# Kernel optimization log

Hardware: AMD Instinct MI355X
Metric: run time of the kernel (lower is better)

The kernel has to match this reference:

```python
import jax, jax.numpy as jnp
import numpy as np

B, S, H, OUT, STEPS = 64, 1024, 512, 256, 32


def setup_inputs() -> dict:
    key = jax.random.key(0)
    ks = jax.random.split(key, 10)
    s = 0.02
    return {
        "encoder_outputs": jax.random.normal(ks[0], (B, S, H), jnp.float32),
        "hidden": jax.random.normal(ks[1], (B, H), jnp.float32),
        # Attention: nn.Linear(2H, 1)
        "attn_w": jax.random.normal(ks[2], (2 * H,), jnp.float32) * s,
        "attn_b": jax.random.normal(ks[3], (1,), jnp.float32) * s,
        # LSTMCell(OUT + H, H): torch gate order i, f, g, o
        "w_ih": jax.random.normal(ks[4], (4 * H, OUT + H), jnp.float32) * s,
        "w_hh": jax.random.normal(ks[5], (4 * H, H), jnp.float32) * s,
        "b_ih": jax.random.normal(ks[6], (4 * H,), jnp.float32) * s,
        "b_hh": jax.random.normal(ks[7], (4 * H,), jnp.float32) * s,
        # fc: nn.Linear(H, OUT)
        "fc_w": jax.random.normal(ks[8], (OUT, H), jnp.float32) * s,
        "fc_b": jax.random.normal(ks[9], (OUT,), jnp.float32) * s,
    }


def reference(encoder_outputs, hidden, attn_w, attn_b, w_ih, w_hh, b_ih, b_hh, fc_w, fc_b):
    # Split attention weight: Linear(concat(enc, hid)) == enc@wa_e + hid@wa_d + b
    wa_e, wa_d = attn_w[:H], attn_w[H:]
    # encoder contribution to attention energy is step-invariant: [B, S]
    enc_energy = jnp.einsum("bsh,h->bs", encoder_outputs, wa_e) + attn_b[0]
    bias = b_ih + b_hh  # [4H]

    def step(carry, _):
        h, c, dec_in = carry
        # Bahdanau-style energy and context
        energy = enc_energy + (h @ wa_d)[:, None]          # [B, S]
        weights = jax.nn.softmax(energy, axis=1)
        context = jnp.einsum("bs,bsh->bh", weights, encoder_outputs)
        # LSTMCell (torch gate order i, f, g, o)
        x = jnp.concatenate([dec_in, context], axis=1)     # [B, OUT+H]
        gates = x @ w_ih.T + h @ w_hh.T + bias             # [B, 4H]
        i, f, g, o = jnp.split(gates, 4, axis=1)
        c_new = jax.nn.sigmoid(f) * c + jax.nn.sigmoid(i) * jnp.tanh(g)
        h_new = jax.nn.sigmoid(o) * jnp.tanh(c_new)
        dec_new = h_new @ fc_w.T + fc_b                    # [B, OUT]
        return (h_new, c_new, dec_new), dec_new

    dec0 = jnp.zeros((encoder_outputs.shape[0], fc_w.shape[0]), encoder_outputs.dtype)
    c0 = jnp.zeros_like(hidden)
    _, outs = jax.lax.scan(step, (hidden, c0, dec0), None, length=STEPS)
    return jnp.transpose(outs, (1, 0, 2))  # [B, STEPS, OUT]
```

## Files before the change

### kernel.cpp

```cpp
#include <hip/hip_runtime.h>
#include <math.h>

#define B 64
#define S 1024
#define H 512
#define OUT 256
#define STEPS 32
#define NG 2048
#define X 768

typedef __attribute__((ext_vector_type(8))) short short8;
typedef __attribute__((ext_vector_type(4))) short s16x4;
typedef __attribute__((ext_vector_type(4))) float f32x4;
typedef __attribute__((ext_vector_type(4))) unsigned u32x4;

__device__ __forceinline__ float sigf(float x) { return 1.0f / (1.0f + __expf(-x)); }
__device__ __forceinline__ float tanhf_fast(float x) {
  return 2.0f / (1.0f + __expf(-2.0f * x)) - 1.0f;
}

__device__ __forceinline__ short f2bf(float x) {
  union { float f; unsigned u; } a; a.f = x;
  unsigned r = a.u + 0x7fffu + ((a.u >> 16) & 1u);
  return (short)(r >> 16);
}
__device__ __forceinline__ float bf2f(short s) {
  union { unsigned u; float f; } a; a.u = ((unsigned)(unsigned short)s) << 16;
  return a.f;
}

__device__ __forceinline__ unsigned load_u32_cg(const unsigned* p) {
  unsigned r;
  asm volatile("global_load_dword %0, %1, off sc0 sc1\n\ts_waitcnt vmcnt(0)"
               : "=v"(r) : "v"(p) : "memory");
  return r;
}

__global__ __launch_bounds__(256) void k_pre(
    const float* __restrict__ enc, const float* __restrict__ attn_w,
    float* __restrict__ part_ctx, float* __restrict__ part_ml,
    const float* __restrict__ w_ih, const float* __restrict__ w_hh,
    const float* __restrict__ fc_w, short* __restrict__ whi,
    short* __restrict__ wlo) {
  __shared__ float sm_acc[4][H];
  __shared__ float sm_m[4], sm_l[4];
  const int cid = blockIdx.x;
  if (cid < 512) {
    const int b = cid >> 3, chunk = cid & 7;
    const int wave = threadIdx.x >> 6, lane = threadIdx.x & 63;
    const float4 wa0 = *(const float4*)(attn_w + lane * 8);
    const float4 wa1 = *(const float4*)(attn_w + lane * 8 + 4);
    const float* eb = enc + (long)b * S * H;
    float m = -1e30f, l = 0.0f;
    float acc[8];
#pragma unroll
    for (int r = 0; r < 8; ++r) acc[r] = 0.0f;
    for (int i = 0; i < 32; ++i) {
      const int s = chunk * 128 + i * 4 + wave;
      const float* row = eb + (long)s * H + lane * 8;
      const float4 v0 = *(const float4*)row;
      const float4 v1 = *(const float4*)(row + 4);
      float e = v0.x * wa0.x + v0.y * wa0.y + v0.z * wa0.z + v0.w * wa0.w +
                v1.x * wa1.x + v1.y * wa1.y + v1.z * wa1.z + v1.w * wa1.w;
#pragma unroll
      for (int msk = 1; msk < 64; msk <<= 1) e += __shfl_xor(e, msk, 64);
      const float mn = fmaxf(m, e);
      const float sc = __expf(m - mn);
      const float p = __expf(e - mn);
      l = l * sc + p;
      m = mn;
      acc[0] = acc[0] * sc + p * v0.x; acc[1] = acc[1] * sc + p * v0.y;
      acc[2] = acc[2] * sc + p * v0.z; acc[3] = acc[3] * sc + p * v0.w;
      acc[4] = acc[4] * sc + p * v1.x; acc[5] = acc[5] * sc + p * v1.y;
      acc[6] = acc[6] * sc + p * v1.z; acc[7] = acc[7] * sc + p * v1.w;
    }
#pragma unroll
    for (int r = 0; r < 8; ++r) sm_acc[wave][lane * 8 + r] = acc[r];
    if (lane == 0) { sm_m[wave] = m; sm_l[wave] = l; }
    __syncthreads();
    const float mb = fmaxf(fmaxf(sm_m[0], sm_m[1]), fmaxf(sm_m[2], sm_m[3]));
    float e0[4];
#pragma unroll
    for (int w = 0; w < 4; ++w) e0[w] = __expf(sm_m[w] - mb);
    const int h0 = threadIdx.x * 2;
    float s0 = 0.f, s1 = 0.f;
#pragma unroll
    for (int w = 0; w < 4; ++w) { s0 += sm_acc[w][h0] * e0[w]; s1 += sm_acc[w][h0 + 1] * e0[w]; }
    float* pc = part_ctx + ((long)chunk * B + b) * H;
    pc[h0] = s0; pc[h0 + 1] = s1;
    if (threadIdx.x == 0) {
      const float lb = sm_l[0] * e0[0] + sm_l[1] * e0[1] + sm_l[2] * e0[2] + sm_l[3] * e0[3];
      part_ml[(chunk * B + b) * 2] = mb;
      part_ml[(chunk * B + b) * 2 + 1] = lb;
    }
  } else {
    const int flat4 = (cid - 512) * 256 + threadIdx.x;
    const int n = flat4 >> 7;
    const int k = (flat4 & 127) << 2;
    const float* wd = w_ih + (long)n * X;
    float v[4] = {0.f, 0.f, 0.f, 0.f};
    for (int j = 0; j < OUT; ++j) {
      const float w = wd[j];
      const float4 f = *(const float4*)(fc_w + (long)j * H + k);
      v[0] = fmaf(w, f.x, v[0]); v[1] = fmaf(w, f.y, v[1]);
      v[2] = fmaf(w, f.z, v[2]); v[3] = fmaf(w, f.w, v[3]);
    }
    const float4 hh = *(const float4*)(w_hh + (long)n * H + k);
    v[0] += hh.x; v[1] += hh.y; v[2] += hh.z; v[3] += hh.w;
    s16x4 hi4, lo4;
#pragma unroll
    for (int e = 0; e < 4; ++e) {
      const short hb = f2bf(v[e]);
      hi4[e] = hb;
      lo4[e] = f2bf(v[e] - bf2f(hb));
    }
    *(s16x4*)(whi + (long)n * H + k) = hi4;
    *(s16x4*)(wlo + (long)n * H + k) = lo4;
  }
}

__global__ __launch_bounds__(256) void k_ctx_reduce(
    const float* __restrict__ part_ctx, const float* __restrict__ part_ml,
    float* __restrict__ ctx) {
  const int b = blockIdx.x;
  float m = -1e30f;
#pragma unroll
  for (int c = 0; c < 8; ++c) m = fmaxf(m, part_ml[(c * B + b) * 2]);
  float L = 0.f, sc[8];
#pragma unroll
  for (int c = 0; c < 8; ++c) {
    sc[c] = __expf(part_ml[(c * B + b) * 2] - m);
    L += part_ml[(c * B + b) * 2 + 1] * sc[c];
  }
  const float inv = 1.0f / L;
  const int h0 = threadIdx.x * 2;
  float s0 = 0.f, s1 = 0.f;
#pragma unroll
  for (int c = 0; c < 8; ++c) {
    const float* pc = part_ctx + ((long)c * B + b) * H;
    s0 += pc[h0] * sc[c]; s1 += pc[h0 + 1] * sc[c];
  }
  ctx[(long)b * H + h0] = s0 * inv;
  ctx[(long)b * H + h0 + 1] = s1 * inv;
}

__global__ __launch_bounds__(256) void k_gbase(
    const float* __restrict__ w_ih, const float* __restrict__ w_hh,
    const float* __restrict__ b_ih, const float* __restrict__ b_hh,
    const float* __restrict__ fc_b, const float* __restrict__ ctx,
    const float* __restrict__ hidden, float* __restrict__ gates0,
    float* __restrict__ gbase2) {
  __shared__ float wt[128][33];
  __shared__ float rb[16][524];
  __shared__ float sfc[256];
  const int n0 = blockIdx.x * 32, b0 = blockIdx.y * 16;
  const int tid = threadIdx.x;
  const int n_l = tid & 31, bh = tid >> 5;
  const int n = n0 + n_l;

  for (int i = tid; i < 16 * 128; i += 256) {
    const int r = i >> 7, c = (i & 127) << 2;
    *(float4*)&rb[r][c] = *(const float4*)(ctx + (long)(b0 + r) * H + c);
  }
  sfc[tid] = fc_b[tid];

  float a1a = 0.f, a1b = 0.f;
  for (int kc = 0; kc < 4; ++kc) {
    __syncthreads();
    for (int i = tid; i < 4096; i += 256) {
      const int r = i >> 7, c = i & 127;
      wt[c][r] = w_ih[(long)(n0 + r) * X + OUT + kc * 128 + c];
    }
    __syncthreads();
#pragma unroll 8
    for (int k = 0; k < 128; ++k) {
      const float wv = wt[k][n_l];
      a1a = fmaf(wv, rb[bh][kc * 128 + k], a1a);
      a1b = fmaf(wv, rb[bh + 8][kc * 128 + k], a1b);
    }
  }

  float db = 0.f;
  for (int kc = 0; kc < 2; ++kc) {
    __syncthreads();
    for (int i = tid; i < 4096; i += 256) {
      const int r = i >> 7, c = i & 127;
      wt[c][r] = w_ih[(long)(n0 + r) * X + kc * 128 + c];
    }
    __syncthreads();
#pragma unroll 8
    for (int k = 0; k < 128; ++k) db = fmaf(wt[k][n_l], sfc[kc * 128 + k], db);
  }

  __syncthreads();
  for (int i = tid; i < 16 * 128; i += 256) {
    const int r = i >> 7, c = (i & 127) << 2;
    *(float4*)&rb[r][c] = *(const float4*)(hidden + (long)(b0 + r) * H + c);
  }
  float a2a = 0.f, a2b = 0.f;
  for (int kc = 0; kc < 4; ++kc) {
    __syncthreads();
    for (int i = tid; i < 4096; i += 256) {
      const int r = i >> 7, c = i & 127;
      wt[c][r] = w_hh[(long)(n0 + r) * H + kc * 128 + c];
    }
    __syncthreads();
#pragma unroll 8
    for (int k = 0; k < 128; ++k) {
      const float wv = wt[k][n_l];
      a2a = fmaf(wv, rb[bh][kc * 128 + k], a2a);
      a2b = fmaf(wv, rb[bh + 8][kc * 128 + k], a2b);
    }
  }

  const float bias = b_ih[n] + b_hh[n];
  gates0[(long)(b0 + bh) * NG + n]     = a1a + bias + a2a;
  gates0[(long)(b0 + bh + 8) * NG + n] = a1b + bias + a2b;
  gbase2[(long)(b0 + bh) * NG + n]     = a1a + bias + db;
  gbase2[(long)(b0 + bh + 8) * NG + n] = a1b + bias + db;
}

#define HSTR 520
__global__ __launch_bounds__(256, 1) void k_recur3(
    const short* __restrict__ whi, const short* __restrict__ wlo,
    const float* __restrict__ gb2, const float* __restrict__ gates0,
    unsigned* __restrict__ hsbf, unsigned int* __restrict__ bar) {
  __shared__ short sh_hi[16 * HSTR];
  __shared__ short sh_lo[16 * HSTR];
  __shared__ float sG[4][8][20];
  __shared__ float sgb[8][64];
  __shared__ float scell[8][16];
  __shared__ int s_fast;

  const int blk = blockIdx.x;
  const int bg = blk & 7;
  const int slice = blk >> 3;
  const int b8 = bg << 3;
  const int hc0 = slice << 4;
  const int tid = threadIdx.x;
  const int w = tid >> 6, l = tid & 63;
  const int ln = l & 15, lk = l >> 4;

  if (tid == 0) {
    unsigned xcc;
    asm volatile("s_getreg_b32 %0, hwreg(20, 0, 32)" : "=s"(xcc));
    __hip_atomic_fetch_or(&bar[7936 + bg], 1u << (xcc & 0xFu),
                          __ATOMIC_RELEASE, __HIP_MEMORY_SCOPE_AGENT);
    unsigned* gbar = &bar[7944 + bg];
    __hip_atomic_fetch_add(gbar, 1u, __ATOMIC_RELEASE, __HIP_MEMORY_SCOPE_AGENT);
    while (load_u32_cg(gbar) < 32u) __builtin_amdgcn_s_sleep(1);
    const unsigned mask = __hip_atomic_load(&bar[7936 + bg], __ATOMIC_ACQUIRE,
                                            __HIP_MEMORY_SCOPE_AGENT);
    s_fast = (__popc(mask) == 1) ? 1 : 0;
  }
  __syncthreads();
  const bool fast = (s_fast != 0);

  for (int i = tid; i < 16 * HSTR; i += 256) { sh_hi[i] = 0; sh_lo[i] = 0; }

  for (int idx = tid; idx < 512; idx += 256) {
    const int b = idx >> 6, gr = idx & 63, g = gr >> 4, j = gr & 15;
    sgb[b][gr] = gb2[(long)(b8 + b) * NG + (g << 9) + hc0 + j];
  }

  short8 wh[16], wl[16];
  {
    const long wb = (long)((w << 9) + hc0 + ln) * H + (lk << 3);
#pragma unroll
    for (int kk = 0; kk < 16; ++kk) {
      wh[kk] = *(const short8*)(whi + wb + kk * 32);
      wl[kk] = *(const short8*)(wlo + wb + kk * 32);
    }
  }
  __syncthreads();

  if (tid < 128) {
    const int b = tid >> 4, j = tid & 15;
    const float* g0 = gates0 + (long)(b8 + b) * NG + hc0 + j;
    const float gi = g0[0];
    const float gg = g0[1024];
    const float go = g0[1536];
    const float cn = sigf(gi) * tanhf_fast(gg);
    const float hn = sigf(go) * tanhf_fast(cn);
    scell[b][j] = cn;
    const short hi = f2bf(hn);
    const short lo = f2bf(hn - bf2f(hi));
    hsbf[(long)(b8 + b) * H + hc0 + j] =
        (unsigned)(unsigned short)hi | ((unsigned)(unsigned short)lo << 16);
  }
  __syncthreads();
  {
    unsigned* flags = bar + bg * 32;
    if (fast) {
      if (tid == 0)
        __hip_atomic_fetch_add(&flags[slice], 1u, __ATOMIC_RELAXED,
                               __HIP_MEMORY_SCOPE_AGENT);
      if (tid < 64) {
        while (!__all(load_u32_cg(flags + (tid & 31)) != 0u)) {}
      }
    } else {
      if (tid == 0)
        __hip_atomic_fetch_add(&flags[slice], 1u, __ATOMIC_RELEASE,
                               __HIP_MEMORY_SCOPE_AGENT);
      if (tid < 64) {
        while (!__all(load_u32_cg(flags + (tid & 31)) != 0u)) {}
      }
      if (tid == 0)
        (void)__hip_atomic_load(&flags[0], __ATOMIC_ACQUIRE,
                                __HIP_MEMORY_SCOPE_AGENT);
    }
    __syncthreads();
  }

  for (int t = 1; t < STEPS; ++t) {
    const unsigned* hb = hsbf + (long)(t - 1) * B * H + (long)b8 * H;
#pragma unroll
    for (int q = 0; q < 4; ++q) {
      const int d0 = q * 1024 + tid * 4;
      const u32x4 v = *(const u32x4*)(hb + d0);
      const int row = d0 >> 9, col = d0 & 511;
      s16x4 hi4, lo4;
#pragma unroll
      for (int e = 0; e < 4; ++e) {
        hi4[e] = (short)(v[e] & 0xFFFFu);
        lo4[e] = (short)(v[e] >> 16);
      }
      *(s16x4*)&sh_hi[row * HSTR + col] = hi4;
      *(s16x4*)&sh_lo[row * HSTR + col] = lo4;
    }
    __syncthreads();

    f32x4 a0 = {0.f, 0.f, 0.f, 0.f};
    f32x4 a1 = {0.f, 0.f, 0.f, 0.f};
    f32x4 a2 = {0.f, 0.f, 0.f, 0.f};
    asm volatile("s_nop 3" ::);
    const int abase = ln * HSTR + (lk << 3);
#pragma unroll
    for (int kk = 0; kk < 16; ++kk) {
      const short8 ah = *(const short8*)&sh_hi[abase + kk * 32];
      const short8 al = *(const short8*)&sh_lo[abase + kk * 32];
      asm volatile("v_mfma_f32_16x16x32_bf16 %0, %1, %2, %0"
                   : "+v"(a0) : "v"(ah), "a"(wh[kk]));
      asm volatile("v_mfma_f32_16x16x32_bf16 %0, %1, %2, %0"
                   : "+v"(a1) : "v"(al), "a"(wh[kk]));
      asm volatile("v_mfma_f32_16x16x32_bf16 %0, %1, %2, %0"
                   : "+v"(a2) : "v"(ah), "a"(wl[kk]));
    }
    asm volatile("s_nop 7\n\ts_nop 7" ::);
    if (lk < 2) {
#pragma unroll
      for (int r = 0; r < 4; ++r)
        sG[w][(lk << 2) + r][ln] = a0[r] + a1[r] + a2[r];
    }
    __syncthreads();

    if (tid < 128) {
      const int b = tid >> 4, j = tid & 15;
      const float gi = sG[0][b][j] + sgb[b][j];
      const float gf = sG[1][b][j] + sgb[b][16 + j];
      const float gg = sG[2][b][j] + sgb[b][32 + j];
      const float go = sG[3][b][j] + sgb[b][48 + j];
      const float c_old = scell[b][j];
      const float cn = sigf(gf) * c_old + sigf(gi) * tanhf_fast(gg);
      const float hn = sigf(go) * tanhf_fast(cn);
      scell[b][j] = cn;
      const short hi = f2bf(hn);
      const short lo = f2bf(hn - bf2f(hi));
      hsbf[(long)t * B * H + (long)(b8 + b) * H + hc0 + j] =
          (unsigned)(unsigned short)hi | ((unsigned)(unsigned short)lo << 16);
    }
    __syncthreads();

    if (t < STEPS - 1) {
      unsigned* flags = bar + t * 256 + bg * 32;
      if (fast) {
        if (tid == 0)
          __hip_atomic_fetch_add(&flags[slice], 1u, __ATOMIC_RELAXED,
                                 __HIP_MEMORY_SCOPE_AGENT);
        if (tid < 64) {
          while (!__all(load_u32_cg(flags + (tid & 31)) != 0u)) {}
        }
      } else {
        if (tid == 0)
          __hip_atomic_fetch_add(&flags[slice], 1u, __ATOMIC_RELEASE,
                                 __HIP_MEMORY_SCOPE_AGENT);
        if (tid < 64) {
          while (!__all(load_u32_cg(flags + (tid & 31)) != 0u)) {}
        }
        if (tid == 0)
          (void)__hip_atomic_load(&flags[0], __ATOMIC_ACQUIRE,
                                  __HIP_MEMORY_SCOPE_AGENT);
      }
      __syncthreads();
    }
  }
}

__global__ __launch_bounds__(256) void k_dec2(
    const unsigned* __restrict__ hsbf, const float* __restrict__ fc_w,
    const float* __restrict__ fc_b, float* __restrict__ out) {
  __shared__ float A[32 * 68];
  __shared__ float Bm[64 * 68];
  const int m0 = blockIdx.x * 32;
  const int o0 = blockIdx.y * 64;
  const int tid = threadIdx.x;
  const int tn = tid & 15, tm = tid >> 4;
  float acc[2][4] = {{0.f, 0.f, 0.f, 0.f}, {0.f, 0.f, 0.f, 0.f}};
  for (int k0 = 0; k0 < H; k0 += 64) {
    for (int idx = tid; idx < 512; idx += 256) {
      const int r = idx >> 4, k4 = idx & 15;
      const u32x4 v = *(const u32x4*)&hsbf[(long)(m0 + r) * H + k0 + k4 * 4];
#pragma unroll
      for (int e = 0; e < 4; ++e)
        A[r * 68 + k4 * 4 + e] =
            bf2f((short)(v[e] & 0xFFFFu)) + bf2f((short)(v[e] >> 16));
    }
    for (int idx = tid; idx < 1024; idx += 256) {
      const int r = idx >> 4, k4 = idx & 15;
      *(float4*)&Bm[r * 68 + k4 * 4] =
          *(const float4*)&fc_w[(long)(o0 + r) * H + k0 + k4 * 4];
    }
    __syncthreads();
#pragma unroll
    for (int k4 = 0; k4 < 16; ++k4) {
      const float4 a0 = *(float4*)&A[tm * 68 + k4 * 4];
      const float4 a1 = *(float4*)&A[(tm + 16) * 68 + k4 * 4];
      const float4 b0 = *(float4*)&Bm[tn * 68 + k4 * 4];
      const float4 b1 = *(float4*)&Bm[(tn + 16) * 68 + k4 * 4];
      const float4 b2 = *(float4*)&Bm[(tn + 32) * 68 + k4 * 4];
      const float4 b3 = *(float4*)&Bm[(tn + 48) * 68 + k4 * 4];
      acc[0][0] += a0.x * b0.x + a0.y * b0.y + a0.z * b0.z + a0.w * b0.w;
      acc[0][1] += a0.x * b1.x + a0.y * b1.y + a0.z * b1.z + a0.w * b1.w;
      acc[0][2] += a0.x * b2.x + a0.y * b2.y + a0.z * b2.z + a0.w * b2.w;
      acc[0][3] += a0.x * b3.x + a0.y * b3.y + a0.z * b3.z + a0.w * b3.w;
      acc[1][0] += a1.x * b0.x + a1.y * b0.y + a1.z * b0.z + a1.w * b0.w;
      acc[1][1] += a1.x * b1.x + a1.y * b1.y + a1.z * b1.z + a1.w * b1.w;
      acc[1][2] += a1.x * b2.x + a1.y * b2.y + a1.z * b2.z + a1.w * b2.w;
      acc[1][3] += a1.x * b3.x + a1.y * b3.y + a1.z * b3.z + a1.w * b3.w;
    }
    __syncthreads();
  }
#pragma unroll
  for (int i = 0; i < 2; ++i) {
    const int m = m0 + tm + 16 * i;
    const int t = m >> 6, b = m & 63;
#pragma unroll
    for (int j = 0; j < 4; ++j) {
      const int o = o0 + tn + 16 * j;
      out[((long)b * STEPS + t) * OUT + o] = acc[i][j] + fc_b[o];
    }
  }
}

extern "C" void kernel_launch(void* const* d_in, const int* in_sizes, int n_in,
                              void* d_out, int out_size, void* d_ws, size_t ws_size,
                              hipStream_t stream) {
  const float* enc = (const float*)d_in[0];
  const float* hidden = (const float*)d_in[1];
  const float* attn_w = (const float*)d_in[2];
  const float* w_ih = (const float*)d_in[4];
  const float* w_hh = (const float*)d_in[5];
  const float* b_ih = (const float*)d_in[6];
  const float* b_hh = (const float*)d_in[7];
  const float* fc_w = (const float*)d_in[8];
  const float* fc_b = (const float*)d_in[9];
  float* out = (float*)d_out;

  float* ws = (float*)d_ws;
  float* ctx      = ws;
  float* part_ctx = ctx + 32768;
  float* part_ml  = part_ctx + 262144;
  short* whi      = (short*)(part_ml + 1024);
  short* wlo      = whi + 1048576;
  float* gates0   = (float*)(wlo + 1048576);
  float* gbase2   = gates0 + 131072;
  unsigned* hsbf  = (unsigned*)(gbase2 + 131072);
  unsigned int* bar = (unsigned int*)(hsbf + 1048576);

  hipMemsetAsync(bar, 0, 7952 * sizeof(unsigned int), stream);
  k_pre<<<1536, 256, 0, stream>>>(enc, attn_w, part_ctx, part_ml,
                                  w_ih, w_hh, fc_w, whi, wlo);
  k_ctx_reduce<<<64, 256, 0, stream>>>(part_ctx, part_ml, ctx);
  k_gbase<<<dim3(64, 4), 256, 0, stream>>>(w_ih, w_hh, b_ih, b_hh, fc_b, ctx,
                                           hidden, gates0, gbase2);

  const short* whi_p = whi;
  const short* wlo_p = wlo;
  const float* gbase2_p = gbase2;
  const float* gates0_p = gates0;
  unsigned* hsbf_p = hsbf;
  unsigned int* bar_p = bar;
  void* kargs[] = {(void*)&whi_p, (void*)&wlo_p, (void*)&gbase2_p,
                   (void*)&gates0_p, (void*)&hsbf_p, (void*)&bar_p};
  hipLaunchCooperativeKernel(reinterpret_cast<const void*>(k_recur3), dim3(256),
                             dim3(256), kargs, 0, stream);

  k_dec2<<<dim3(64, 4), 256, 0, stream>>>(hsbf, fc_w, fc_b, out);
}
```

Measured before the change: 246.2 us.

## Tile weight-fold GEMM through LDS and fuse context reduction into gbase

The weight-folding half of k_pre now loads each fc_w tile into shared memory once per block and reuses it across 8 gate rows with 16 accumulators per thread. Before, every thread streamed fc_w from global memory on its own with scalar w_ih loads. The separate k_ctx_reduce kernel is removed; k_gbase now merges the per-chunk softmax partials itself while building its ctx tile, which saves one launch and the ctx round trip. In exchange, k_pre uses about 41KB of shared memory, which may lower occupancy for its attention blocks, and each k_gbase block redoes the reduction for its own batch rows.

```diff
diff --git a/kernel.cpp b/kernel.cpp
--- a/kernel.cpp
+++ b/kernel.cpp
@@ -42,12 +42,15 @@
     const float* __restrict__ w_ih, const float* __restrict__ w_hh,
     const float* __restrict__ fc_w, short* __restrict__ whi,
     short* __restrict__ wlo) {
-  __shared__ float sm_acc[4][H];
-  __shared__ float sm_m[4], sm_l[4];
+  __shared__ float smem[10336];
   const int cid = blockIdx.x;
+  const int tid = threadIdx.x;
   if (cid < 512) {
+    float* sm_acc = smem;
+    float* sm_m = smem + 2048;
+    float* sm_l = smem + 2052;
     const int b = cid >> 3, chunk = cid & 7;
-    const int wave = threadIdx.x >> 6, lane = threadIdx.x & 63;
+    const int wave = tid >> 6, lane = tid & 63;
     const float4 wa0 = *(const float4*)(attn_w + lane * 8);
     const float4 wa1 = *(const float4*)(attn_w + lane * 8 + 4);
     const float* eb = enc + (long)b * S * H;
@@ -75,94 +78,127 @@
       acc[6] = acc[6] * sc + p * v1.z; acc[7] = acc[7] * sc + p * v1.w;
     }
 #pragma unroll
-    for (int r = 0; r < 8; ++r) sm_acc[wave][lane * 8 + r] = acc[r];
+    for (int r = 0; r < 8; ++r) sm_acc[wave * 512 + lane * 8 + r] = acc[r];
     if (lane == 0) { sm_m[wave] = m; sm_l[wave] = l; }
     __syncthreads();
     const float mb = fmaxf(fmaxf(sm_m[0], sm_m[1]), fmaxf(sm_m[2], sm_m[3]));
     float e0[4];
 #pragma unroll
     for (int w = 0; w < 4; ++w) e0[w] = __expf(sm_m[w] - mb);
-    const int h0 = threadIdx.x * 2;
+    const int h0 = tid * 2;
     float s0 = 0.f, s1 = 0.f;
 #pragma unroll
-    for (int w = 0; w < 4; ++w) { s0 += sm_acc[w][h0] * e0[w]; s1 += sm_acc[w][h0 + 1] * e0[w]; }
+    for (int w = 0; w < 4; ++w) {
+      s0 += sm_acc[w * 512 + h0] * e0[w];
+      s1 += sm_acc[w * 512 + h0 + 1] * e0[w];
+    }
     float* pc = part_ctx + ((long)chunk * B + b) * H;
     pc[h0] = s0; pc[h0 + 1] = s1;
-    if (threadIdx.x == 0) {
+    if (tid == 0) {
       const float lb = sm_l[0] * e0[0] + sm_l[1] * e0[1] + sm_l[2] * e0[2] + sm_l[3] * e0[3];
       part_ml[(chunk * B + b) * 2] = mb;
       part_ml[(chunk * B + b) * 2 + 1] = lb;
     }
   } else {
-    const int flat4 = (cid - 512) * 256 + threadIdx.x;
-    const int n = flat4 >> 7;
-    const int k = (flat4 & 127) << 2;
-    const float* wd = w_ih + (long)n * X;
-    float v[4] = {0.f, 0.f, 0.f, 0.f};
-    for (int j = 0; j < OUT; ++j) {
-      const float w = wd[j];
-      const float4 f = *(const float4*)(fc_w + (long)j * H + k);
-      v[0] = fmaf(w, f.x, v[0]); v[1] = fmaf(w, f.y, v[1]);
-      v[2] = fmaf(w, f.z, v[2]); v[3] = fmaf(w, f.w, v[3]);
-    }
-    const float4 hh = *(const float4*)(w_hh + (long)n * H + k);
-    v[0] += hh.x; v[1] += hh.y; v[2] += hh.z; v[3] += hh.w;
-    s16x4 hi4, lo4;
-#pragma unroll
-    for (int e = 0; e < 4; ++e) {
-      const short hb = f2bf(v[e]);
-      hi4[e] = hb;
-      lo4[e] = f2bf(v[e] - bf2f(hb));
-    }
-    *(s16x4*)(whi + (long)n * H + k) = hi4;
-    *(s16x4*)(wlo + (long)n * H + k) = lo4;
-  }
-}
-
-__global__ __launch_bounds__(256) void k_ctx_reduce(
-    const float* __restrict__ part_ctx, const float* __restrict__ part_ml,
-    float* __restrict__ ctx) {
-  const int b = blockIdx.x;
-  float m = -1e30f;
-#pragma unroll
-  for (int c = 0; c < 8; ++c) m = fmaxf(m, part_ml[(c * B + b) * 2]);
-  float L = 0.f, sc[8];
-#pragma unroll
-  for (int c = 0; c < 8; ++c) {
-    sc[c] = __expf(part_ml[(c * B + b) * 2] - m);
-    L += part_ml[(c * B + b) * 2 + 1] * sc[c];
-  }
-  const float inv = 1.0f / L;
-  const int h0 = threadIdx.x * 2;
-  float s0 = 0.f, s1 = 0.f;
-#pragma unroll
-  for (int c = 0; c < 8; ++c) {
-    const float* pc = part_ctx + ((long)c * B + b) * H;
-    s0 += pc[h0] * sc[c]; s1 += pc[h0 + 1] * sc[c];
-  }
-  ctx[(long)b * H + h0] = s0 * inv;
-  ctx[(long)b * H + h0 + 1] = s1 * inv;
+    float* ft = smem;
+    float* wd = smem + 8256;
+    const int n0 = (cid - 512) * 8;
+    for (int i = tid; i < 512; i += 256) {
+      const int r = i >> 6, c4 = (i & 63) << 2;
+      *(float4*)&wd[r * 260 + c4] = *(const float4*)(w_ih + (long)(n0 + r) * X + c4);
+    }
+    float acc[16];
+#pragma unroll
+    for (int e = 0; e < 16; ++e) acc[e] = 0.f;
+    const int n_l = tid >> 5, kq = tid & 31;
+    for (int jt = 0; jt < 16; ++jt) {
+      __syncthreads();
+      for (int i = tid; i < 2048; i += 256) {
+        const int r = i >> 7, c4 = (i & 127) << 2;
+        *(float4*)&ft[r * 516 + c4] =
+            *(const float4*)(fc_w + (long)(jt * 16 + r) * H + c4);
+      }
+      __syncthreads();
+#pragma unroll 4
+      for (int j = 0; j < 16; ++j) {
+        const float w = wd[n_l * 260 + jt * 16 + j];
+#pragma unroll
+        for (int e4 = 0; e4 < 4; ++e4) {
+          const float4 f = *(float4*)&ft[j * 516 + kq * 4 + e4 * 128];
+          acc[e4 * 4 + 0] = fmaf(w, f.x, acc[e4 * 4 + 0]);
+          acc[e4 * 4 + 1] = fmaf(w, f.y, acc[e4 * 4 + 1]);
+          acc[e4 * 4 + 2] = fmaf(w, f.z, acc[e4 * 4 + 2]);
+          acc[e4 * 4 + 3] = fmaf(w, f.w, acc[e4 * 4 + 3]);
+        }
+      }
+    }
+    const long rbase = (long)(n0 + n_l) * H;
+#pragma unroll
+    for (int e4 = 0; e4 < 4; ++e4) {
+      const int k = kq * 4 + e4 * 128;
+      const float4 hh = *(const float4*)(w_hh + rbase + k);
+      float v[4] = {acc[e4 * 4] + hh.x, acc[e4 * 4 + 1] + hh.y,
+                    acc[e4 * 4 + 2] + hh.z, acc[e4 * 4 + 3] + hh.w};
+      s16x4 hi4, lo4;
+#pragma unroll
+      for (int e = 0; e < 4; ++e) {
+        const short hb = f2bf(v[e]);
+        hi4[e] = hb;
+        lo4[e] = f2bf(v[e] - bf2f(hb));
+      }
+      *(s16x4*)(whi + rbase + k) = hi4;
+      *(s16x4*)(wlo + rbase + k) = lo4;
+    }
+  }
 }
 
 __global__ __launch_bounds__(256) void k_gbase(
     const float* __restrict__ w_ih, const float* __restrict__ w_hh,
     const float* __restrict__ b_ih, const float* __restrict__ b_hh,
-    const float* __restrict__ fc_b, const float* __restrict__ ctx,
-    const float* __restrict__ hidden, float* __restrict__ gates0,
-    float* __restrict__ gbase2) {
+    const float* __restrict__ fc_b, const float* __restrict__ part_ctx,
+    const float* __restrict__ part_ml, const float* __restrict__ hidden,
+    float* __restrict__ gates0, float* __restrict__ gbase2) {
   __shared__ float wt[128][33];
   __shared__ float rb[16][524];
   __shared__ float sfc[256];
+  __shared__ float sf[16][8];
   const int n0 = blockIdx.x * 32, b0 = blockIdx.y * 16;
   const int tid = threadIdx.x;
   const int n_l = tid & 31, bh = tid >> 5;
   const int n = n0 + n_l;
 
+  if (tid < 16) {
+    const int r = tid;
+    float ml[8], ll[8];
+    float m = -1e30f;
+#pragma unroll
+    for (int c = 0; c < 8; ++c) {
+      ml[c] = part_ml[(c * B + b0 + r) * 2];
+      ll[c] = part_ml[(c * B + b0 + r) * 2 + 1];
+      m = fmaxf(m, ml[c]);
+    }
+    float L = 0.f;
+#pragma unroll
+    for (int c = 0; c < 8; ++c) L += ll[c] * __expf(ml[c] - m);
+    const float inv = 1.0f / L;
+#pragma unroll
+    for (int c = 0; c < 8; ++c) sf[r][c] = __expf(ml[c] - m) * inv;
+  }
+  sfc[tid] = fc_b[tid];
+  __syncthreads();
+
   for (int i = tid; i < 16 * 128; i += 256) {
-    const int r = i >> 7, c = (i & 127) << 2;
-    *(float4*)&rb[r][c] = *(const float4*)(ctx + (long)(b0 + r) * H + c);
-  }
-  sfc[tid] = fc_b[tid];
+    const int r = i >> 7, c4 = (i & 127) << 2;
+    float4 s = {0.f, 0.f, 0.f, 0.f};
+#pragma unroll
+    for (int c8 = 0; c8 < 8; ++c8) {
+      const float4 p = *(const float4*)(part_ctx + ((long)c8 * B + b0 + r) * H + c4);
+      const float f = sf[r][c8];
+      s.x = fmaf(p.x, f, s.x); s.y = fmaf(p.y, f, s.y);
+      s.z = fmaf(p.z, f, s.z); s.w = fmaf(p.w, f, s.w);
+    }
+    *(float4*)&rb[r][c4] = s;
+  }
 
   float a1a = 0.f, a1b = 0.f;
   for (int kc = 0; kc < 4; ++kc) {
@@ -467,8 +503,7 @@
   float* out = (float*)d_out;
 
   float* ws = (float*)d_ws;
-  float* ctx      = ws;
-  float* part_ctx = ctx + 32768;
+  float* part_ctx = ws;
   float* part_ml  = part_ctx + 262144;
   short* whi      = (short*)(part_ml + 1024);
   short* wlo      = whi + 1048576;
@@ -478,11 +513,11 @@
   unsigned int* bar = (unsigned int*)(hsbf + 1048576);
 
   hipMemsetAsync(bar, 0, 7952 * sizeof(unsigned int), stream);
-  k_pre<<<1536, 256, 0, stream>>>(enc, attn_w, part_ctx, part_ml,
-                                  w_ih, w_hh, fc_w, whi, wlo);
-  k_ctx_reduce<<<64, 256, 0, stream>>>(part_ctx, part_ml, ctx);
-  k_gbase<<<dim3(64, 4), 256, 0, stream>>>(w_ih, w_hh, b_ih, b_hh, fc_b, ctx,
-                                           hidden, gates0, gbase2);
+  k_pre<<<768, 256, 0, stream>>>(enc, attn_w, part_ctx, part_ml,
+                                 w_ih, w_hh, fc_w, whi, wlo);
+  k_gbase<<<dim3(64, 4), 256, 0, stream>>>(w_ih, w_hh, b_ih, b_hh, fc_b,
+                                           part_ctx, part_ml, hidden,
+                                           gates0, gbase2);
 
   const short* whi_p = whi;
   const short* wlo_p = wlo;
```

New measurement: 242.1 us. No clear change (-1.6%).
